# Optimization experiments

Measured on AMD Instinct MI355X. Metric: run time of the kernel, lower is better.

The kernel has to match this reference:

```python
import jax, jax.numpy as jnp
import numpy as np

N_NODES = 50000
IN_CH = 128
HIDDEN = 64
HEADS = 2
OUT_CH = 40
N_EDGES = 800000
NEG_SLOPE = 0.2


def gat_layer(x, src, dst, W, att_src, att_dst, bias, concat):
    # x: [N, F_in]; src/dst: [E] (self-loops already appended)
    N = x.shape[0]
    H, C = att_src.shape
    h = (x @ W).reshape(N, H, C)                      # [N, H, C]
    a_s = (h * att_src[None]).sum(-1)                 # [N, H]
    a_d = (h * att_dst[None]).sum(-1)                 # [N, H]
    e = jax.nn.leaky_relu(a_s[src] + a_d[dst], NEG_SLOPE)   # [E, H]
    # numerically-stable segment softmax over incoming edges per dst node
    m = jax.ops.segment_max(e, dst, num_segments=N)   # [N, H]
    m = jnp.where(jnp.isfinite(m), m, 0.0)
    m = jax.lax.stop_gradient(m)
    ex = jnp.exp(e - m[dst])                          # [E, H]
    denom = jax.ops.segment_sum(ex, dst, num_segments=N)    # [N, H]
    alpha = ex / (denom[dst] + 1e-16)                 # [E, H]
    out = jax.ops.segment_sum(alpha[:, :, None] * h[src], dst, num_segments=N)  # [N, H, C]
    out = out.reshape(N, H * C) if concat else out.mean(axis=1)
    return out + bias


def setup_inputs() -> dict:
    key = jax.random.key(0)
    ks = jax.random.split(key, 10)
    node_feat = jax.random.normal(ks[0], (N_NODES, IN_CH), dtype=jnp.float32)
    edge_index = jax.random.randint(ks[1], (2, N_EDGES), 0, N_NODES, dtype=jnp.int64)
    s1 = 1.0 / np.sqrt(IN_CH)
    s2 = 1.0 / np.sqrt(HIDDEN * HEADS)
    return {
        "node_feat": node_feat,
        "edge_index": edge_index,
        "W1": jax.random.normal(ks[2], (IN_CH, HEADS * HIDDEN), dtype=jnp.float32) * s1,
        "att_src1": jax.random.normal(ks[3], (HEADS, HIDDEN), dtype=jnp.float32) * s1,
        "att_dst1": jax.random.normal(ks[4], (HEADS, HIDDEN), dtype=jnp.float32) * s1,
        "b1": jnp.zeros((HEADS * HIDDEN,), dtype=jnp.float32),
        "W2": jax.random.normal(ks[5], (HEADS * HIDDEN, OUT_CH), dtype=jnp.float32) * s2,
        "att_src2": jax.random.normal(ks[6], (1, OUT_CH), dtype=jnp.float32) * s2,
        "att_dst2": jax.random.normal(ks[7], (1, OUT_CH), dtype=jnp.float32) * s2,
        "b2": jnp.zeros((OUT_CH,), dtype=jnp.float32),
    }


def reference(node_feat, edge_index, W1, att_src1, att_dst1, b1, W2, att_src2, att_dst2, b2):
    N = node_feat.shape[0]
    loop = jnp.arange(N, dtype=edge_index.dtype)
    src = jnp.concatenate([edge_index[0], loop])  # add self loops (PyG default)
    dst = jnp.concatenate([edge_index[1], loop])
    # eval mode: dropout is identity; use_bn=False
    x = gat_layer(node_feat, src, dst, W1, att_src1, att_dst1, b1, concat=True)
    x = jax.nn.elu(x)
    x = gat_layer(x, src, dst, W2, att_src2, att_dst2, b2, concat=False)
    return x
```

## Files before the change

### kernel.cpp

```cpp
#include <hip/hip_runtime.h>
#include <hip/hip_bf16.h>

#define N_NODES 50000
#define E0      800000
#define E_TOT   850000

typedef short short8 __attribute__((ext_vector_type(8)));
typedef float floatx4 __attribute__((ext_vector_type(4)));

__device__ __forceinline__ float lrelu(float x) { return x > 0.f ? x : 0.2f * x; }

__device__ __forceinline__ unsigned short f2bf(float f) {
    unsigned int u = __float_as_uint(f);
    u += 0x7fffu + ((u >> 16) & 1u);
    return (unsigned short)(u >> 16);
}
__device__ __forceinline__ float lo_bf(unsigned int p) { return __uint_as_float(p << 16); }
__device__ __forceinline__ float hi_bf(unsigned int p) { return __uint_as_float(p & 0xffff0000u); }

__device__ __forceinline__ short8 pack_bf16x8(float4 a, float4 b) {
    short8 r;
    r[0] = (short)f2bf(a.x); r[1] = (short)f2bf(a.y); r[2] = (short)f2bf(a.z); r[3] = (short)f2bf(a.w);
    r[4] = (short)f2bf(b.x); r[5] = (short)f2bf(b.y); r[6] = (short)f2bf(b.z); r[7] = (short)f2bf(b.w);
    return r;
}

__device__ __forceinline__ void fma8(float2* A, float w, uint4 h) {
    A[0].x += w * lo_bf(h.x); A[0].y += w * hi_bf(h.x);
    A[1].x += w * lo_bf(h.y); A[1].y += w * hi_bf(h.y);
    A[2].x += w * lo_bf(h.z); A[2].y += w * hi_bf(h.z);
    A[3].x += w * lo_bf(h.w); A[3].y += w * hi_bf(h.w);
}

__global__ __launch_bounds__(256) void hist_w(const int* __restrict__ ei, int* __restrict__ ghist,
                                              const float* __restrict__ W1, const float* __restrict__ W2,
                                              unsigned short* __restrict__ Wt1, unsigned short* __restrict__ Wt2) {
    __shared__ int h[256];
    int b = blockIdx.x, t = threadIdx.x;
    h[t] = 0;
    int i = b * 256 + t;
    if (i < 128 * 128) {
        int nn = i >> 7, k = i & 127;
        Wt1[i] = f2bf(W1[k * 128 + nn]);
    } else if (i < 128 * 128 + 48 * 128) {
        int j = i - 128 * 128;
        int nn = j >> 7, k = j & 127;
        Wt2[j] = (nn < 40) ? f2bf(W2[k * 40 + nn]) : (unsigned short)0;
    }
    __syncthreads();
    int base = b * 3328;
    #pragma unroll
    for (int k = 0; k < 13; ++k) {
        int e = base + t + k * 256;
        if (e < E_TOT) {
            int dst = (e < E0) ? ei[E0 + e] : (e - E0);
            atomicAdd(&h[dst >> 8], 1);
        }
    }
    __syncthreads();
    ghist[t * 256 + b] = h[t];
}

__global__ __launch_bounds__(256) void scan_local(const int* __restrict__ src, int* __restrict__ dst,
                                                  int* __restrict__ bsum, int n) {
    __shared__ int wsum[4];
    int t = threadIdx.x, lane = t & 63, wid = t >> 6;
    int idx = blockIdx.x * 1024 + t * 4;
    int4 v = make_int4(0, 0, 0, 0);
    if (idx < n) v = *reinterpret_cast<const int4*>(src + idx);
    int tsum = v.x + v.y + v.z + v.w;
    int sc = tsum;
    #pragma unroll
    for (int s = 1; s < 64; s <<= 1) {
        int up = __shfl_up(sc, s);
        if (lane >= s) sc += up;
    }
    if (lane == 63) wsum[wid] = sc;
    __syncthreads();
    int woff = 0;
    for (int w = 0; w < wid; ++w) woff += wsum[w];
    int b0 = woff + (sc - tsum);
    if (idx < n) {
        int4 o;
        o.x = b0;
        o.y = b0 + v.x;
        o.z = b0 + v.x + v.y;
        o.w = b0 + v.x + v.y + v.z;
        *reinterpret_cast<int4*>(dst + idx) = o;
    }
    if (t == 255) bsum[blockIdx.x] = woff + sc;
}

__global__ __launch_bounds__(256) void scan_addoff(int* __restrict__ arr, const int* __restrict__ bsum,
                                                   int* __restrict__ total, int n, int nb) {
    __shared__ int add_sh;
    int t = threadIdx.x;
    if (t < 64) {
        int v = (t < nb) ? bsum[t] : 0;
        int sc = v;
        #pragma unroll
        for (int s = 1; s < 64; s <<= 1) {
            int up = __shfl_up(sc, s);
            if (t >= s) sc += up;
        }
        if (t == (int)blockIdx.x) add_sh = sc - v;
        if (blockIdx.x == 0 && t == nb - 1) total[0] = sc;
    }
    __syncthreads();
    int idx = blockIdx.x * 1024 + t * 4;
    if (idx < n) {
        int add = add_sh;
        int4 v4 = *reinterpret_cast<int4*>(arr + idx);
        v4.x += add; v4.y += add; v4.z += add; v4.w += add;
        *reinterpret_cast<int4*>(arr + idx) = v4;
    }
}

__global__ __launch_bounds__(256) void scatter1(const int* __restrict__ ei, const int* __restrict__ gbase,
                                                unsigned int* __restrict__ tmpk) {
    __shared__ int cur[256];
    int b = blockIdx.x, t = threadIdx.x;
    cur[t] = gbase[t * 256 + b];
    __syncthreads();
    int base = b * 3328;
    #pragma unroll
    for (int k = 0; k < 13; ++k) {
        int e = base + t + k * 256;
        if (e < E_TOT) {
            int src, dst;
            if (e < E0) { src = ei[e]; dst = ei[E0 + e]; }
            else        { src = dst = e - E0; }
            int pos = atomicAdd(&cur[dst >> 8], 1);
            tmpk[pos] = ((unsigned)dst << 16) | (unsigned)src;
        }
    }
}

__global__ __launch_bounds__(256) void sort_bucket(const unsigned int* __restrict__ tmpk,
                                                   const int* __restrict__ gbase,
                                                   unsigned int* __restrict__ keys, int* __restrict__ offs) {
    __shared__ unsigned int skey[8192];
    __shared__ unsigned int sorted[8192];
    __shared__ int h2[256], binb[256], cur2[256];
    int q = blockIdx.x, t = threadIdx.x;
    int start = gbase[q * 256];
    int end   = gbase[(q + 1) * 256];
    int n = end - start;
    if (n > 8192) n = 8192;
    h2[t] = 0;
    __syncthreads();
    for (int i = t; i < n; i += 256) {
        unsigned int k = tmpk[start + i];
        skey[i] = k;
        atomicAdd(&h2[(k >> 16) & 255], 1);
    }
    __syncthreads();
    if (t < 64) {
        int carry = 0;
        #pragma unroll
        for (int ch = 0; ch < 4; ++ch) {
            int idx = ch * 64 + t;
            int v = h2[idx];
            int sc = v;
            #pragma unroll
            for (int s = 1; s < 64; s <<= 1) {
                int up = __shfl_up(sc, s);
                if (t >= s) sc += up;
            }
            binb[idx] = sc - v + carry;
            cur2[idx] = sc - v + carry;
            carry += __shfl(sc, 63);
        }
    }
    __syncthreads();
    for (int i = t; i < n; i += 256) {
        unsigned int k = skey[i];
        int pos = atomicAdd(&cur2[(k >> 16) & 255], 1);
        sorted[pos] = k;
    }
    __syncthreads();
    for (int i = t; i < n; i += 256) keys[start + i] = sorted[i];
    int idx = q * 256 + t;
    if (idx <= N_NODES) offs[idx] = start + binb[t];
}

__global__ __launch_bounds__(256) void edge_w1(const unsigned int* __restrict__ keys,
                                               const float* __restrict__ a_s, const float* __restrict__ a_d,
                                               float2* __restrict__ w1) {
    int e = blockIdx.x * 256 + threadIdx.x;
    if (e >= E_TOT) return;
    unsigned int k = keys[e];
    int src = k & 0xFFFF, dst = k >> 16;
    float2 av = *reinterpret_cast<const float2*>(&a_s[src * 2]);
    float2 dv = *reinterpret_cast<const float2*>(&a_d[dst * 2]);
    float2 w;
    w.x = __expf(lrelu(av.x + dv.x));
    w.y = __expf(lrelu(av.y + dv.y));
    w1[e] = w;
}

__global__ __launch_bounds__(256) void gemm1_mfma(const float* __restrict__ X, const unsigned short* __restrict__ Wt,
                                                  const float* __restrict__ asw, const float* __restrict__ adw,
                                                  unsigned short* __restrict__ h1b, float* __restrict__ a_s,
                                                  float* __restrict__ a_d, int nRows) {
    int t = threadIdx.x, lane = t & 63, wave = t >> 6;
    int l15 = lane & 15, g = lane >> 4;
    int r0 = blockIdx.x * 64;
    int row = r0 + wave * 16 + l15;
    bool rv = row < nRows;
    const float* xrow = X + (size_t)(rv ? row : 0) * 128;

    float asv[8], adv[8];
    #pragma unroll
    for (int nt = 0; nt < 8; ++nt) { asv[nt] = asw[nt * 16 + l15]; adv[nt] = adw[nt * 16 + l15]; }

    floatx4 acc[8];
    #pragma unroll
    for (int nt = 0; nt < 8; ++nt) acc[nt] = (floatx4){0.f, 0.f, 0.f, 0.f};

    #pragma unroll
    for (int ks = 0; ks < 4; ++ks) {
        float4 xa = *reinterpret_cast<const float4*>(xrow + ks * 32 + g * 8);
        float4 xb = *reinterpret_cast<const float4*>(xrow + ks * 32 + g * 8 + 4);
        short8 af = pack_bf16x8(xa, xb);
        #pragma unroll
        for (int nt = 0; nt < 8; ++nt) {
            short8 bf = *reinterpret_cast<const short8*>(Wt + (size_t)(nt * 16 + l15) * 128 + ks * 32 + g * 8);
            acc[nt] = __builtin_amdgcn_mfma_f32_16x16x32_bf16(af, bf, acc[nt], 0, 0, 0);
        }
    }

    #pragma unroll
    for (int i = 0; i < 4; ++i) {
        int gr = r0 + wave * 16 + g * 4 + i;
        float s0 = 0.f, d0 = 0.f, s1 = 0.f, d1 = 0.f;
        #pragma unroll
        for (int nt = 0; nt < 4; ++nt) { s0 += acc[nt][i] * asv[nt]; d0 += acc[nt][i] * adv[nt]; }
        #pragma unroll
        for (int nt = 4; nt < 8; ++nt) { s1 += acc[nt][i] * asv[nt]; d1 += acc[nt][i] * adv[nt]; }
        #pragma unroll
        for (int sh = 1; sh < 16; sh <<= 1) {
            s0 += __shfl_xor(s0, sh); d0 += __shfl_xor(d0, sh);
            s1 += __shfl_xor(s1, sh); d1 += __shfl_xor(d1, sh);
        }
        if (gr < nRows) {
            if (l15 == 0) {
                a_s[gr * 2] = s0;     a_d[gr * 2] = d0;
                a_s[gr * 2 + 1] = s1; a_d[gr * 2 + 1] = d1;
            }
            #pragma unroll
            for (int nt = 0; nt < 8; ++nt)
                h1b[(size_t)gr * 128 + nt * 16 + l15] = f2bf(acc[nt][i]);
        }
    }
}

__global__ __launch_bounds__(256) void gemm2_mfma(const unsigned short* __restrict__ X2b,
                                                  const unsigned short* __restrict__ Wt,
                                                  const float* __restrict__ asw, const float* __restrict__ adw,
                                                  unsigned short* __restrict__ h2b, float* __restrict__ a_s,
                                                  float* __restrict__ a_d, int nRows) {
    int t = threadIdx.x, lane = t & 63, wave = t >> 6;
    int l15 = lane & 15, g = lane >> 4;
    int r0 = blockIdx.x * 64;
    int row = r0 + wave * 16 + l15;
    bool rv = row < nRows;
    const unsigned short* xrow = X2b + (size_t)(rv ? row : 0) * 128;

    float asv[3], adv[3];
    #pragma unroll
    for (int nt = 0; nt < 3; ++nt) {
        int col = nt * 16 + l15;
        asv[nt] = (col < 40) ? asw[col] : 0.f;
        adv[nt] = (col < 40) ? adw[col] : 0.f;
    }

    floatx4 acc[3];
    #pragma unroll
    for (int nt = 0; nt < 3; ++nt) acc[nt] = (floatx4){0.f, 0.f, 0.f, 0.f};

    #pragma unroll
    for (int ks = 0; ks < 4; ++ks) {
        short8 af = *reinterpret_cast<const short8*>(xrow + ks * 32 + g * 8);
        #pragma unroll
        for (int nt = 0; nt < 3; ++nt) {
            short8 bf = *reinterpret_cast<const short8*>(Wt + (size_t)(nt * 16 + l15) * 128 + ks * 32 + g * 8);
            acc[nt] = __builtin_amdgcn_mfma_f32_16x16x32_bf16(af, bf, acc[nt], 0, 0, 0);
        }
    }

    #pragma unroll
    for (int i = 0; i < 4; ++i) {
        int gr = r0 + wave * 16 + g * 4 + i;
        float ps = 0.f, pd = 0.f;
        #pragma unroll
        for (int nt = 0; nt < 3; ++nt) { ps += acc[nt][i] * asv[nt]; pd += acc[nt][i] * adv[nt]; }
        #pragma unroll
        for (int sh = 1; sh < 16; sh <<= 1) { ps += __shfl_xor(ps, sh); pd += __shfl_xor(pd, sh); }
        if (gr < nRows) {
            if (l15 == 0) { a_s[gr] = ps; a_d[gr] = pd; }
            #pragma unroll
            for (int nt = 0; nt < 3; ++nt) {
                int col = nt * 16 + l15;
                if (col < 40) h2b[(size_t)gr * 40 + col] = f2bf(acc[nt][i]);
            }
        }
    }
}

__global__ __launch_bounds__(256) void aggregate1(const unsigned short* __restrict__ Hb,
                                                  const float2* __restrict__ w1, const int* __restrict__ offs,
                                                  const unsigned int* __restrict__ keys, const float* __restrict__ bias,
                                                  unsigned short* __restrict__ X2b, int n) {
    int t = threadIdx.x, lane = t & 63, wid = t >> 6;
    int node = blockIdx.x * 4 + wid;
    if (node >= n) return;
    int c = lane & 15, q = lane >> 4, head = c >> 3;
    int beg = offs[node], deg = offs[node + 1] - beg;
    float den = 0.f;
    float2 acc0[4], acc1[4];
    #pragma unroll
    for (int m = 0; m < 4; ++m) { acc0[m] = make_float2(0.f, 0.f); acc1[m] = make_float2(0.f, 0.f); }

    for (int j = 0; j < deg; j += 8) {
        int j0 = j + q, j1 = j + 4 + q;
        int s0 = 0, s1 = 0;
        float wh0 = 0.f, wh1 = 0.f;
        if (j0 < deg) {
            s0 = keys[beg + j0] & 0xFFFF;
            float2 W0 = w1[beg + j0];
            wh0 = head ? W0.y : W0.x;
        }
        if (j1 < deg) {
            s1 = keys[beg + j1] & 0xFFFF;
            float2 W1v = w1[beg + j1];
            wh1 = head ? W1v.y : W1v.x;
        }
        uint4 h0 = *reinterpret_cast<const uint4*>(&Hb[(size_t)s0 * 128 + c * 8]);
        uint4 h1 = *reinterpret_cast<const uint4*>(&Hb[(size_t)s1 * 128 + c * 8]);
        den += wh0 + wh1;
        fma8(acc0, wh0, h0);
        fma8(acc1, wh1, h1);
    }
    #pragma unroll
    for (int m = 0; m < 4; ++m) { acc0[m].x += acc1[m].x; acc0[m].y += acc1[m].y; }
    den += __shfl_xor(den, 16); den += __shfl_xor(den, 32);
    #pragma unroll
    for (int m = 0; m < 4; ++m) {
        acc0[m].x += __shfl_xor(acc0[m].x, 16); acc0[m].x += __shfl_xor(acc0[m].x, 32);
        acc0[m].y += __shfl_xor(acc0[m].y, 16); acc0[m].y += __shfl_xor(acc0[m].y, 32);
    }
    if (q == 0) {
        float dinv = 1.f / (den + 1e-16f);
        float4 b0 = *reinterpret_cast<const float4*>(&bias[c * 8]);
        float4 b1 = *reinterpret_cast<const float4*>(&bias[c * 8 + 4]);
        float va[8] = {acc0[0].x, acc0[0].y, acc0[1].x, acc0[1].y, acc0[2].x, acc0[2].y, acc0[3].x, acc0[3].y};
        float bb[8] = {b0.x, b0.y, b0.z, b0.w, b1.x, b1.y, b1.z, b1.w};
        float o[8];
        #pragma unroll
        for (int k = 0; k < 8; ++k) {
            float v = va[k] * dinv + bb[k];
            o[k] = v > 0.f ? v : (__expf(v) - 1.f);
        }
        uint4 pk;
        pk.x = (unsigned)f2bf(o[0]) | ((unsigned)f2bf(o[1]) << 16);
        pk.y = (unsigned)f2bf(o[2]) | ((unsigned)f2bf(o[3]) << 16);
        pk.z = (unsigned)f2bf(o[4]) | ((unsigned)f2bf(o[5]) << 16);
        pk.w = (unsigned)f2bf(o[6]) | ((unsigned)f2bf(o[7]) << 16);
        *reinterpret_cast<uint4*>(&X2b[(size_t)node * 128 + c * 8]) = pk;
    }
}

__global__ __launch_bounds__(256) void aggregate2(const unsigned short* __restrict__ Hb,
                                                  const float* __restrict__ a_s, const float* __restrict__ a_d,
                                                  const int* __restrict__ offs, const unsigned int* __restrict__ keys,
                                                  const float* __restrict__ bias, float* __restrict__ out, int n) {
    int t = threadIdx.x, lane = t & 63, wid = t >> 6;
    int node = blockIdx.x * 4 + wid;
    if (node >= n) return;
    int g = lane / 5, c = lane - g * 5;
    bool dead = (g >= 12);
    if (dead) { g = 0; c = 0; }
    int beg = offs[node], deg = offs[node + 1] - beg;
    float adv = a_d[node];
    float den = 0.f;
    float2 acc0[4], acc1[4];
    #pragma unroll
    for (int m = 0; m < 4; ++m) { acc0[m] = make_float2(0.f, 0.f); acc1[m] = make_float2(0.f, 0.f); }

    for (int j = 0; j < deg; j += 24) {
        int j0 = j + g, j1 = j + 12 + g;
        int s0 = 0, s1 = 0;
        float w0 = 0.f, w1v = 0.f;
        if (!dead && j0 < deg) {
            s0 = keys[beg + j0] & 0xFFFF;
            w0 = __expf(lrelu(a_s[s0] + adv));
        }
        if (!dead && j1 < deg) {
            s1 = keys[beg + j1] & 0xFFFF;
            w1v = __expf(lrelu(a_s[s1] + adv));
        }
        uint4 h0 = *reinterpret_cast<const uint4*>(&Hb[(size_t)s0 * 40 + c * 8]);
        uint4 h1 = *reinterpret_cast<const uint4*>(&Hb[(size_t)s1 * 40 + c * 8]);
        den += w0 + w1v;
        fma8(acc0, w0, h0);
        fma8(acc1, w1v, h1);
    }
    #pragma unroll
    for (int m = 0; m < 4; ++m) { acc0[m].x += acc1[m].x; acc0[m].y += acc1[m].y; }
    den += __shfl(den, lane + 30);
    den += __shfl(den, lane + 15);
    {
        float d5 = __shfl(den, lane + 5), d10 = __shfl(den, lane + 10);
        den = den + d5 + d10;
    }
    #pragma unroll
    for (int m = 0; m < 4; ++m) {
        float ax = acc0[m].x, ay = acc0[m].y;
        ax += __shfl(ax, lane + 30); ay += __shfl(ay, lane + 30);
        ax += __shfl(ax, lane + 15); ay += __shfl(ay, lane + 15);
        float ax5 = __shfl(ax, lane + 5),  ay5 = __shfl(ay, lane + 5);
        float ax10 = __shfl(ax, lane + 10), ay10 = __shfl(ay, lane + 10);
        acc0[m].x = ax + ax5 + ax10;
        acc0[m].y = ay + ay5 + ay10;
    }
    if (lane < 5) {
        float dinv = 1.f / (den + 1e-16f);
        float4 b0 = *reinterpret_cast<const float4*>(&bias[c * 8]);
        float4 b1 = *reinterpret_cast<const float4*>(&bias[c * 8 + 4]);
        float4 o0, o1;
        o0.x = acc0[0].x * dinv + b0.x; o0.y = acc0[0].y * dinv + b0.y;
        o0.z = acc0[1].x * dinv + b0.z; o0.w = acc0[1].y * dinv + b0.w;
        o1.x = acc0[2].x * dinv + b1.x; o1.y = acc0[2].y * dinv + b1.y;
        o1.z = acc0[3].x * dinv + b1.z; o1.w = acc0[3].y * dinv + b1.w;
        *reinterpret_cast<float4*>(&out[(size_t)node * 40 + c * 8])     = o0;
        *reinterpret_cast<float4*>(&out[(size_t)node * 40 + c * 8 + 4]) = o1;
    }
}

extern "C" void kernel_launch(void* const* d_in, const int* in_sizes, int n_in,
                              void* d_out, int out_size, void* d_ws, size_t ws_size,
                              hipStream_t stream) {
    (void)in_sizes; (void)n_in; (void)out_size; (void)ws_size;
    const float* x    = (const float*)d_in[0];
    const int*   ei   = (const int*)d_in[1];
    const float* W1   = (const float*)d_in[2];
    const float* as1w = (const float*)d_in[3];
    const float* ad1w = (const float*)d_in[4];
    const float* b1   = (const float*)d_in[5];
    const float* W2   = (const float*)d_in[6];
    const float* as2w = (const float*)d_in[7];
    const float* ad2w = (const float*)d_in[8];
    const float* b2   = (const float*)d_in[9];
    float* out = (float*)d_out;

    float* ws = (float*)d_ws;
    float* h1slot = ws; ws += (size_t)N_NODES * 128;
    float* x2slot = ws; ws += (size_t)N_NODES * 128;
    float* a_s1 = ws; ws += N_NODES * 2;
    float* a_d1 = ws; ws += N_NODES * 2;
    float* a_s2 = ws; ws += N_NODES;
    float* a_d2 = ws; ws += N_NODES;
    float* h2slot = ws; ws += (size_t)N_NODES * 40;
    int* offs  = (int*)ws;
    int* ghist = offs + 50432;
    int* gbase = ghist + 65536;
    int* bsum  = gbase + 65536;
    int* total = bsum + 64;
    unsigned int* tmpk = (unsigned int*)(total + 4);
    unsigned int* keys = tmpk + E_TOT;
    float2* w1 = (float2*)(keys + E_TOT);
    unsigned short* Wt1 = (unsigned short*)(w1 + E_TOT);
    unsigned short* Wt2 = Wt1 + 128 * 128;

    unsigned short* h1b = (unsigned short*)h1slot;
    unsigned short* x2b = (unsigned short*)x2slot;
    unsigned short* h2b = (unsigned short*)h2slot;

    const int EBLK = (E_TOT + 255) / 256;

    hist_w<<<256, 256, 0, stream>>>(ei, ghist, W1, W2, Wt1, Wt2);
    scan_local<<<64, 256, 0, stream>>>(ghist, gbase, bsum, 65536);
    scan_addoff<<<64, 256, 0, stream>>>(gbase, bsum, total, 65536, 64);
    scatter1<<<256, 256, 0, stream>>>(ei, gbase, tmpk);
    sort_bucket<<<196, 256, 0, stream>>>(tmpk, gbase, keys, offs);
    gemm1_mfma<<<(N_NODES + 63) / 64, 256, 0, stream>>>(x, Wt1, as1w, ad1w, h1b, a_s1, a_d1, N_NODES);
    edge_w1<<<EBLK, 256, 0, stream>>>(keys, a_s1, a_d1, w1);
    aggregate1<<<(N_NODES + 3) / 4, 256, 0, stream>>>(h1b, w1, offs, keys, b1, x2b, N_NODES);
    gemm2_mfma<<<(N_NODES + 63) / 64, 256, 0, stream>>>(x2b, Wt2, as2w, ad2w, h2b, a_s2, a_d2, N_NODES);
    aggregate2<<<(N_NODES + 3) / 4, 256, 0, stream>>>(h2b, a_s2, a_d2, offs, keys, b2, out, N_NODES);
}
```

Measured before the change: 137.2 us.

## Fuse edge softmax weights into bucket sort and pack key/weights per edge

The edge_w1 kernel is folded into the bucket-sort kernel, which now runs after gemm1 and writes a 16-byte record per edge holding the key and both head exp-weights. This removes one launch and a re-read of the keys array. aggregate1 reads that single record instead of separate keys and weight arrays, and its loop now processes 16 edges per iteration with four independent feature gathers in flight. In exchange, per-edge storage grows from 12 to 16 bytes, and the sort now has to wait for gemm1 before it can run.

Result: no change. 138.4 us (+0.9%).

```diff
diff --git a/kernel.cpp b/kernel.cpp
--- a/kernel.cpp
+++ b/kernel.cpp
@@ -136,9 +136,11 @@
     }
 }
 
-__global__ __launch_bounds__(256) void sort_bucket(const unsigned int* __restrict__ tmpk,
-                                                   const int* __restrict__ gbase,
-                                                   unsigned int* __restrict__ keys, int* __restrict__ offs) {
+__global__ __launch_bounds__(256) void sort_w(const unsigned int* __restrict__ tmpk,
+                                              const int* __restrict__ gbase,
+                                              const float* __restrict__ a_s, const float* __restrict__ a_d,
+                                              unsigned int* __restrict__ keys, uint4* __restrict__ ew,
+                                              int* __restrict__ offs) {
     __shared__ unsigned int skey[8192];
     __shared__ unsigned int sorted[8192];
     __shared__ int h2[256], binb[256], cur2[256];
@@ -179,24 +181,21 @@
         sorted[pos] = k;
     }
     __syncthreads();
-    for (int i = t; i < n; i += 256) keys[start + i] = sorted[i];
+    for (int i = t; i < n; i += 256) {
+        unsigned int k = sorted[i];
+        keys[start + i] = k;
+        int src = k & 0xFFFF, dst = k >> 16;
+        float2 av = *reinterpret_cast<const float2*>(&a_s[src * 2]);
+        float2 dv = *reinterpret_cast<const float2*>(&a_d[dst * 2]);
+        uint4 e;
+        e.x = k;
+        e.y = __float_as_uint(__expf(lrelu(av.x + dv.x)));
+        e.z = __float_as_uint(__expf(lrelu(av.y + dv.y)));
+        e.w = 0;
+        ew[start + i] = e;
+    }
     int idx = q * 256 + t;
     if (idx <= N_NODES) offs[idx] = start + binb[t];
-}
-
-__global__ __launch_bounds__(256) void edge_w1(const unsigned int* __restrict__ keys,
-                                               const float* __restrict__ a_s, const float* __restrict__ a_d,
-                                               float2* __restrict__ w1) {
-    int e = blockIdx.x * 256 + threadIdx.x;
-    if (e >= E_TOT) return;
-    unsigned int k = keys[e];
-    int src = k & 0xFFFF, dst = k >> 16;
-    float2 av = *reinterpret_cast<const float2*>(&a_s[src * 2]);
-    float2 dv = *reinterpret_cast<const float2*>(&a_d[dst * 2]);
-    float2 w;
-    w.x = __expf(lrelu(av.x + dv.x));
-    w.y = __expf(lrelu(av.y + dv.y));
-    w1[e] = w;
 }
 
 __global__ __launch_bounds__(256) void gemm1_mfma(const float* __restrict__ X, const unsigned short* __restrict__ Wt,
@@ -309,8 +308,8 @@
 }
 
 __global__ __launch_bounds__(256) void aggregate1(const unsigned short* __restrict__ Hb,
-                                                  const float2* __restrict__ w1, const int* __restrict__ offs,
-                                                  const unsigned int* __restrict__ keys, const float* __restrict__ bias,
+                                                  const uint4* __restrict__ ew, const int* __restrict__ offs,
+                                                  const float* __restrict__ bias,
                                                   unsigned short* __restrict__ X2b, int n) {
     int t = threadIdx.x, lane = t & 63, wid = t >> 6;
     int node = blockIdx.x * 4 + wid;
@@ -322,25 +321,27 @@
     #pragma unroll
     for (int m = 0; m < 4; ++m) { acc0[m] = make_float2(0.f, 0.f); acc1[m] = make_float2(0.f, 0.f); }
 
-    for (int j = 0; j < deg; j += 8) {
-        int j0 = j + q, j1 = j + 4 + q;
-        int s0 = 0, s1 = 0;
-        float wh0 = 0.f, wh1 = 0.f;
-        if (j0 < deg) {
-            s0 = keys[beg + j0] & 0xFFFF;
-            float2 W0 = w1[beg + j0];
-            wh0 = head ? W0.y : W0.x;
-        }
-        if (j1 < deg) {
-            s1 = keys[beg + j1] & 0xFFFF;
-            float2 W1v = w1[beg + j1];
-            wh1 = head ? W1v.y : W1v.x;
-        }
-        uint4 h0 = *reinterpret_cast<const uint4*>(&Hb[(size_t)s0 * 128 + c * 8]);
-        uint4 h1 = *reinterpret_cast<const uint4*>(&Hb[(size_t)s1 * 128 + c * 8]);
-        den += wh0 + wh1;
-        fma8(acc0, wh0, h0);
-        fma8(acc1, wh1, h1);
+    for (int j = 0; j < deg; j += 16) {
+        int sE[4]; float wE[4];
+        #pragma unroll
+        for (int k2 = 0; k2 < 4; ++k2) {
+            int idx = j + 4 * k2 + q;
+            sE[k2] = 0; wE[k2] = 0.f;
+            if (idx < deg) {
+                uint4 e = ew[beg + idx];
+                sE[k2] = (int)(e.x & 0xFFFF);
+                wE[k2] = __uint_as_float(head ? e.z : e.y);
+            }
+        }
+        uint4 h0 = *reinterpret_cast<const uint4*>(&Hb[(size_t)sE[0] * 128 + c * 8]);
+        uint4 h1 = *reinterpret_cast<const uint4*>(&Hb[(size_t)sE[1] * 128 + c * 8]);
+        uint4 h2 = *reinterpret_cast<const uint4*>(&Hb[(size_t)sE[2] * 128 + c * 8]);
+        uint4 h3 = *reinterpret_cast<const uint4*>(&Hb[(size_t)sE[3] * 128 + c * 8]);
+        den += wE[0] + wE[1] + wE[2] + wE[3];
+        fma8(acc0, wE[0], h0);
+        fma8(acc1, wE[1], h1);
+        fma8(acc0, wE[2], h2);
+        fma8(acc1, wE[3], h3);
     }
     #pragma unroll
     for (int m = 0; m < 4; ++m) { acc0[m].x += acc1[m].x; acc0[m].y += acc1[m].y; }
@@ -469,24 +470,21 @@
     int* total = bsum + 64;
     unsigned int* tmpk = (unsigned int*)(total + 4);
     unsigned int* keys = tmpk + E_TOT;
-    float2* w1 = (float2*)(keys + E_TOT);
-    unsigned short* Wt1 = (unsigned short*)(w1 + E_TOT);
+    uint4* ew = (uint4*)(keys + E_TOT);
+    unsigned short* Wt1 = (unsigned short*)(ew + E_TOT);
     unsigned short* Wt2 = Wt1 + 128 * 128;
 
     unsigned short* h1b = (unsigned short*)h1slot;
     unsigned short* x2b = (unsigned short*)x2slot;
     unsigned short* h2b = (unsigned short*)h2slot;
-
-    const int EBLK = (E_TOT + 255) / 256;
 
     hist_w<<<256, 256, 0, stream>>>(ei, ghist, W1, W2, Wt1, Wt2);
     scan_local<<<64, 256, 0, stream>>>(ghist, gbase, bsum, 65536);
     scan_addoff<<<64, 256, 0, stream>>>(gbase, bsum, total, 65536, 64);
     scatter1<<<256, 256, 0, stream>>>(ei, gbase, tmpk);
-    sort_bucket<<<196, 256, 0, stream>>>(tmpk, gbase, keys, offs);
     gemm1_mfma<<<(N_NODES + 63) / 64, 256, 0, stream>>>(x, Wt1, as1w, ad1w, h1b, a_s1, a_d1, N_NODES);
-    edge_w1<<<EBLK, 256, 0, stream>>>(keys, a_s1, a_d1, w1);
-    aggregate1<<<(N_NODES + 3) / 4, 256, 0, stream>>>(h1b, w1, offs, keys, b1, x2b, N_NODES);
+    sort_w<<<196, 256, 0, stream>>>(tmpk, gbase, a_s1, a_d1, keys, ew, offs);
+    aggregate1<<<(N_NODES + 3) / 4, 256, 0, stream>>>(h1b, ew, offs, b1, x2b, N_NODES);
     gemm2_mfma<<<(N_NODES + 63) / 64, 256, 0, stream>>>(x2b, Wt2, as2w, ad2w, h2b, a_s2, a_d2, N_NODES);
     aggregate2<<<(N_NODES + 3) / 4, 256, 0, stream>>>(h2b, a_s2, a_d2, offs, keys, b2, out, N_NODES);
 }
```
